# Kernel optimization log

Measured on AMD Instinct MI355X. Metric: run time of the kernel, lower is better.

The kernel has to match this reference:

```python
import jax, jax.numpy as jnp
import numpy as np

N = 1_000_000
DIM = 128
NUM_GRAPHS = 4096


def setup_inputs() -> dict:
    key = jax.random.key(0)
    kx, kq, kb = jax.random.split(key, 3)
    x = jax.random.normal(kx, (N, DIM), dtype=jnp.float32)
    query = jax.random.normal(kq, (DIM,), dtype=jnp.float32) * 0.02
    batch = jnp.sort(jax.random.randint(kb, (N,), 0, NUM_GRAPHS, dtype=jnp.int64))
    return {"x": x, "query": query, "batch": batch}


def reference(x, query, batch):
    # scores: [N] dot of each node feature with the learned query vector
    scores = jnp.einsum("nd,d->n", x, query)
    # segment-wise numerically-stable softmax over nodes belonging to each graph
    seg_max = jax.ops.segment_max(scores, batch, num_segments=NUM_GRAPHS)
    ex = jnp.exp(scores - seg_max[batch])  # [N]
    seg_sum = jax.ops.segment_sum(ex, batch, num_segments=NUM_GRAPHS)
    weights = ex / seg_sum[batch]  # [N]
    # weighted scatter-add pooling -> [num_graphs, dim]
    pooled = jax.ops.segment_sum(weights[:, None] * x, batch, num_segments=NUM_GRAPHS)
    return pooled
```

## Files before the change

kernel.cpp:

```cpp
#include <hip/hip_runtime.h>
#include <math.h>

#define DIM 128
#define CHUNK 8
#define STREAMS 8
#define ROUND (STREAMS * CHUNK)

typedef float v4f __attribute__((ext_vector_type(4)));

__global__ __launch_bounds__(256) void seg_bounds_kernel(
    const int* __restrict__ batch, int* __restrict__ seg, int n, int ng)
{
    const int i = blockIdx.x * blockDim.x + threadIdx.x;
    if (i > n) return;
    const int prev = (i == 0) ? -1 : batch[i - 1];
    const int cur  = (i == n) ? ng : batch[i];
    for (int g = prev + 1; g <= cur; ++g) seg[g] = i;
}

__global__ __launch_bounds__(256) void attnpool_kernel(
    const float* __restrict__ x, const float* __restrict__ q,
    const int* __restrict__ seg, float* __restrict__ out)
{
    const int g    = blockIdx.x;
    const int tid  = threadIdx.x;
    const int wave = tid >> 6;
    const int lane = tid & 63;
    const int half = lane >> 5;
    const int hl   = lane & 31;
    const int sid  = wave * 2 + half;

    const int lo = seg[g];
    const int hi = seg[g + 1];

    const float4 qf = *(const float4*)(q + hl * 4);

    float  m = -INFINITY;
    float  l = 0.f;
    float4 o = make_float4(0.f, 0.f, 0.f, 0.f);

    const int i0 = lo + sid;
    const v4f zz = (v4f)0.f;
    const float* xb = x + hl * 4;

    v4f cur[CHUNK];
    #pragma unroll
    for (int j = 0; j < CHUNK; ++j) {
        const int ii = i0 + j * STREAMS;
        cur[j] = (ii < hi) ? *(const v4f*)(xb + (size_t)ii * DIM) : zz;
    }

    for (int base = i0; base < hi; base += ROUND) {
        v4f nxt[CHUNK];
        #pragma unroll
        for (int j = 0; j < CHUNK; ++j) {
            const int ii = base + ROUND + j * STREAMS;
            nxt[j] = (ii < hi) ? *(const v4f*)(xb + (size_t)ii * DIM) : zz;
        }

        float s[CHUNK];
        #pragma unroll
        for (int j = 0; j < CHUNK; ++j)
            s[j] = cur[j].x * qf.x + cur[j].y * qf.y + cur[j].z * qf.z + cur[j].w * qf.w;

        #pragma unroll
        for (int d = 16; d >= 1; d >>= 1) {
            #pragma unroll
            for (int j = 0; j < CHUNK; ++j)
                s[j] += __shfl_xor(s[j], d);
        }

        #pragma unroll
        for (int j = 0; j < CHUNK; ++j)
            if (base + j * STREAMS >= hi) s[j] = -INFINITY;

        float smax = s[0];
        #pragma unroll
        for (int j = 1; j < CHUNK; ++j) smax = fmaxf(smax, s[j]);

        if (smax > m) {
            const float a = __expf(m - smax);
            l *= a;
            o.x *= a; o.y *= a; o.z *= a; o.w *= a;
            m = smax;
        }

        #pragma unroll
        for (int j = 0; j < CHUNK; ++j) {
            const float p = (base + j * STREAMS < hi) ? __expf(s[j] - m) : 0.f;
            l += p;
            o.x += p * cur[j].x; o.y += p * cur[j].y;
            o.z += p * cur[j].z; o.w += p * cur[j].w;
        }

        #pragma unroll
        for (int j = 0; j < CHUNK; ++j) cur[j] = nxt[j];
    }

    __shared__ float sm_m[STREAMS];
    __shared__ float sm_l[STREAMS];
    __shared__ float sm_o[STREAMS * DIM];
    if (hl == 0) { sm_m[sid] = m; sm_l[sid] = l; }
    *(float4*)(sm_o + sid * DIM + hl * 4) = o;
    __syncthreads();

    if (tid < DIM) {
        float M = -INFINITY;
        #pragma unroll
        for (int h = 0; h < STREAMS; ++h)
            if (sm_l[h] > 0.f && sm_m[h] > M) M = sm_m[h];
        float L = 0.f, O = 0.f;
        #pragma unroll
        for (int h = 0; h < STREAMS; ++h) {
            if (sm_l[h] > 0.f) {
                const float c = __expf(sm_m[h] - M);
                L += c * sm_l[h];
                O += c * sm_o[h * DIM + tid];
            }
        }
        __builtin_nontemporal_store((L > 0.f) ? (O / L) : 0.f, out + (size_t)g * DIM + tid);
    }
}

extern "C" void kernel_launch(void* const* d_in, const int* in_sizes, int n_in,
                              void* d_out, int out_size, void* d_ws, size_t ws_size,
                              hipStream_t stream) {
    const float* x     = (const float*)d_in[0];
    const float* q     = (const float*)d_in[1];
    const int*   batch = (const int*)d_in[2];
    float*       out   = (float*)d_out;
    const int n          = in_sizes[0] / DIM;
    const int num_graphs = out_size / DIM;

    int* seg = (int*)d_ws;
    const int sb = (n + 1 + 255) / 256;
    seg_bounds_kernel<<<sb, 256, 0, stream>>>(batch, seg, n, num_graphs);
    attnpool_kernel<<<num_graphs, 256, 0, stream>>>(x, q, seg, out);
}
```

Before: 650.3 us.

## Assign one half-wave per graph and drop the cross-stream shared-memory merge

Each 32-lane half-wave now owns a whole graph (eight graphs per block) and streams its rows contiguously, where before a block of eight interleaved streams cooperated on one graph. This removes the shared-memory reduction, the __syncthreads barrier and the serial merge done by only 128 threads. Out-of-range loads are clamped to the last valid row instead of being predicated to zero, and the kernel asks for two blocks per CU through launch bounds. The cost is less parallelism per graph: only 512 blocks are launched, and each half-wave walks about 244 rows serially, so there is less memory-level parallelism and load imbalance between graphs can show up.

```diff
diff --git a/kernel.cpp b/kernel.cpp
--- a/kernel.cpp
+++ b/kernel.cpp
@@ -3,8 +3,8 @@
 
 #define DIM 128
 #define CHUNK 8
-#define STREAMS 8
-#define ROUND (STREAMS * CHUNK)
+#define GPB 8
+#define NUM_GRAPHS_EXPECTED 4096
 
 typedef float v4f __attribute__((ext_vector_type(4)));
 
@@ -18,44 +18,43 @@
     for (int g = prev + 1; g <= cur; ++g) seg[g] = i;
 }
 
-__global__ __launch_bounds__(256) void attnpool_kernel(
+__global__ __launch_bounds__(256, 2) void attnpool_kernel(
     const float* __restrict__ x, const float* __restrict__ q,
     const int* __restrict__ seg, float* __restrict__ out)
 {
-    const int g    = blockIdx.x;
     const int tid  = threadIdx.x;
     const int wave = tid >> 6;
     const int lane = tid & 63;
     const int half = lane >> 5;
     const int hl   = lane & 31;
     const int sid  = wave * 2 + half;
+    const int g    = blockIdx.x * GPB + sid;
 
     const int lo = seg[g];
     const int hi = seg[g + 1];
 
     const float4 qf = *(const float4*)(q + hl * 4);
+    const float* xb = x + hl * 4;
 
     float  m = -INFINITY;
     float  l = 0.f;
     float4 o = make_float4(0.f, 0.f, 0.f, 0.f);
 
-    const int i0 = lo + sid;
-    const v4f zz = (v4f)0.f;
-    const float* xb = x + hl * 4;
+    const int safe_last = (hi > lo) ? (hi - 1) : 0;
 
     v4f cur[CHUNK];
     #pragma unroll
     for (int j = 0; j < CHUNK; ++j) {
-        const int ii = i0 + j * STREAMS;
-        cur[j] = (ii < hi) ? *(const v4f*)(xb + (size_t)ii * DIM) : zz;
+        const int ii = (lo + j < hi) ? (lo + j) : safe_last;
+        cur[j] = *(const v4f*)(xb + (size_t)ii * DIM);
     }
 
-    for (int base = i0; base < hi; base += ROUND) {
+    for (int t = lo; t < hi; t += CHUNK) {
         v4f nxt[CHUNK];
         #pragma unroll
         for (int j = 0; j < CHUNK; ++j) {
-            const int ii = base + ROUND + j * STREAMS;
-            nxt[j] = (ii < hi) ? *(const v4f*)(xb + (size_t)ii * DIM) : zz;
+            const int ii = (t + CHUNK + j < hi) ? (t + CHUNK + j) : safe_last;
+            nxt[j] = *(const v4f*)(xb + (size_t)ii * DIM);
         }
 
         float s[CHUNK];
@@ -72,7 +71,7 @@
 
         #pragma unroll
         for (int j = 0; j < CHUNK; ++j)
-            if (base + j * STREAMS >= hi) s[j] = -INFINITY;
+            if (t + j >= hi) s[j] = -INFINITY;
 
         float smax = s[0];
         #pragma unroll
@@ -87,7 +86,7 @@
 
         #pragma unroll
         for (int j = 0; j < CHUNK; ++j) {
-            const float p = (base + j * STREAMS < hi) ? __expf(s[j] - m) : 0.f;
+            const float p = (t + j < hi) ? __expf(s[j] - m) : 0.f;
             l += p;
             o.x += p * cur[j].x; o.y += p * cur[j].y;
             o.z += p * cur[j].z; o.w += p * cur[j].w;
@@ -97,29 +96,10 @@
         for (int j = 0; j < CHUNK; ++j) cur[j] = nxt[j];
     }
 
-    __shared__ float sm_m[STREAMS];
-    __shared__ float sm_l[STREAMS];
-    __shared__ float sm_o[STREAMS * DIM];
-    if (hl == 0) { sm_m[sid] = m; sm_l[sid] = l; }
-    *(float4*)(sm_o + sid * DIM + hl * 4) = o;
-    __syncthreads();
-
-    if (tid < DIM) {
-        float M = -INFINITY;
-        #pragma unroll
-        for (int h = 0; h < STREAMS; ++h)
-            if (sm_l[h] > 0.f && sm_m[h] > M) M = sm_m[h];
-        float L = 0.f, O = 0.f;
-        #pragma unroll
-        for (int h = 0; h < STREAMS; ++h) {
-            if (sm_l[h] > 0.f) {
-                const float c = __expf(sm_m[h] - M);
-                L += c * sm_l[h];
-                O += c * sm_o[h * DIM + tid];
-            }
-        }
-        __builtin_nontemporal_store((L > 0.f) ? (O / L) : 0.f, out + (size_t)g * DIM + tid);
-    }
+    const float inv = (l > 0.f) ? (1.f / l) : 0.f;
+    float4 r;
+    r.x = o.x * inv; r.y = o.y * inv; r.z = o.z * inv; r.w = o.w * inv;
+    *(float4*)(out + (size_t)g * DIM + hl * 4) = r;
 }
 
 extern "C" void kernel_launch(void* const* d_in, const int* in_sizes, int n_in,
@@ -135,5 +115,5 @@
     int* seg = (int*)d_ws;
     const int sb = (n + 1 + 255) / 256;
     seg_bounds_kernel<<<sb, 256, 0, stream>>>(batch, seg, n, num_graphs);
-    attnpool_kernel<<<num_graphs, 256, 0, stream>>>(x, q, seg, out);
+    attnpool_kernel<<<num_graphs / GPB, 256, 0, stream>>>(x, q, seg, out);
 }
```

Result: no change. 659.8 us (+1.5%).
